# Kernel optimization log

Measured on AMD Instinct MI355X. Metric: run time of the kernel, lower is better.

## Reference

```python
import jax, jax.numpy as jnp
import numpy as np

DIM = 33
LAMBDA_SMOOTH = 1e-4
LAMBDA_MN = 10.0


def _tvmn(LUT):
    """TVMN smoothness/monotonicity regularizer on LUT [num,3,d,d,d]."""
    d = DIM
    edge = jnp.array([0, d - 2])
    wr = jnp.ones((d, d, d - 1), jnp.float32).at[..., edge].set(2.0)
    wg = jnp.ones((d, d - 1, d), jnp.float32).at[:, edge, :].set(2.0)
    wb = jnp.ones((d - 1, d, d), jnp.float32).at[edge, :, :].set(2.0)
    dif_r = LUT[..., :-1] - LUT[..., 1:]
    dif_g = LUT[..., :-1, :] - LUT[..., 1:, :]
    dif_b = LUT[..., :-1, :, :] - LUT[..., 1:, :, :]
    t0 = (dif_r ** 2 * wr).mean() + (dif_g ** 2 * wg).mean() + (dif_b ** 2 * wb).mean()
    t1 = ((jax.nn.relu(dif_r * wr)) ** 2).mean() \
       + ((jax.nn.relu(dif_g * wg)) ** 2).mean() \
       + ((jax.nn.relu(dif_b * wb)) ** 2).mean()
    return LAMBDA_SMOOTH * t0 + LAMBDA_MN * t1


def _trilinear_one(lut, img):
    """lut: [3,d,d,d] indexed [c, b_idx, g_idx, r_idx]; img: [3,H,W] in [0,1).
    Matches the CUDA kernel: id = r_id + g_id*dim + b_id*dim^2 per channel."""
    d = DIM
    binsize = 1.000001 / (d - 1)
    r, g, b = img[0], img[1], img[2]
    fr = r / binsize
    fg = g / binsize
    fb = b / binsize
    rid = jnp.floor(fr).astype(jnp.int32)
    gid = jnp.floor(fg).astype(jnp.int32)
    bid = jnp.floor(fb).astype(jnp.int32)
    rd = fr - rid  # fractional parts
    gd = fg - gid
    bd = fb - bid

    def corner(db, dg, dr):
        return lut[:, bid + db, gid + dg, rid + dr]  # [3,H,W]

    out = ((1 - rd) * (1 - gd) * (1 - bd)) * corner(0, 0, 0) \
        + (rd * (1 - gd) * (1 - bd)) * corner(0, 0, 1) \
        + ((1 - rd) * gd * (1 - bd)) * corner(0, 1, 0) \
        + (rd * gd * (1 - bd)) * corner(0, 1, 1) \
        + ((1 - rd) * (1 - gd) * bd) * corner(1, 0, 0) \
        + (rd * (1 - gd) * bd) * corner(1, 0, 1) \
        + ((1 - rd) * gd * bd) * corner(1, 1, 0) \
        + (rd * gd * bd) * corner(1, 1, 1)
    return out  # [3,H,W]


def setup_inputs() -> dict:
    key = jax.random.key(0)
    k1, k2, k3 = jax.random.split(key, 3)
    B, num, d = 4, 20, DIM
    weights = jax.random.normal(k1, (B, num), jnp.float32)
    LUTs = jax.random.normal(k2, (num, 3, d, d, d), jnp.float32) * 0.1
    img_org = jax.random.uniform(k3, (B, 3, 1080, 1920), jnp.float32)
    return {"weights": weights, "LUTs": LUTs, "img_org": img_org}


def reference(weights, LUTs, img_org):
    # CLUT mode '--': D3LUTs = LUTs directly; TVMN regularizer on the bases
    tvmn_loss = _tvmn(LUTs)
    num = LUTs.shape[0]
    # weights.mm(D3LUTs.reshape(num,-1)).reshape(-1,3,d,d,d)
    D3LUT = jnp.einsum('bn,ncijk->bcijk', weights, LUTs)  # [B,3,d,d,d]
    # per-batch LUT trilinear interpolation (lut.shape[0]==x.shape[0] branch)
    img_res = jax.vmap(_trilinear_one)(D3LUT, img_org)  # [B,3,H,W]
    fakes = img_res + img_org
    return (fakes, D3LUT, tvmn_loss)
```

## Files before the change

### kernel.cpp

```cpp
#include <hip/hip_runtime.h>
#include <hip/hip_fp16.h>

#define DIM 33
#define D2  (DIM*DIM)
#define D3  (DIM*DIM*DIM)
#define CH3 (3*D3)
#define NUM 20
#define BATCH 4
#define IMG_H 1080
#define IMG_W 1920
#define HW (IMG_H*IMG_W)
#define FAKES_SIZE (BATCH*3*HW)
#define D3LUT_SIZE (BATCH*CH3)
#define NCELL 32
#define CELLS (NCELL*NCELL*NCELL)
#define TVMN_BLOCKS 2112
#define TEX_BYTES ((size_t)BATCH * CELLS * 32)
#define PX_PER_BLOCK 512
#define TRI_PIX_BLOCKS (BATCH * HW / PX_PER_BLOCK)

typedef unsigned int u32x4 __attribute__((ext_vector_type(4)));

__global__ void mix_tvmn_kernel(const float* __restrict__ w,
                                const float* __restrict__ luts,
                                float* __restrict__ d3lut,
                                float* __restrict__ partials) {
    int t = blockIdx.x * blockDim.x + threadIdx.x;

    if (t < CH3) {
        float a0 = 0.f, a1 = 0.f, a2 = 0.f, a3 = 0.f;
#pragma unroll
        for (int n = 0; n < NUM; ++n) {
            float v = luts[(size_t)n * CH3 + t];
            a0 += w[0 * NUM + n] * v;
            a1 += w[1 * NUM + n] * v;
            a2 += w[2 * NUM + n] * v;
            a3 += w[3 * NUM + n] * v;
        }
        d3lut[(size_t)0 * CH3 + t] = a0;
        d3lut[(size_t)1 * CH3 + t] = a1;
        d3lut[(size_t)2 * CH3 + t] = a2;
        d3lut[(size_t)3 * CH3 + t] = a3;
    }

    const int total = NUM * 3 * D3;
    float s0 = 0.f, s1 = 0.f;
    for (int idx = t; idx < total; idx += gridDim.x * blockDim.x) {
        int k  = idx % DIM;
        int r1 = idx / DIM;
        int j  = r1 % DIM;
        int r2 = r1 / DIM;
        int i  = r2 % DIM;
        float v = luts[idx];
        if (k < DIM - 1) {
            float dif = v - luts[idx + 1];
            float ww = (k == 0 || k == DIM - 2) ? 2.f : 1.f;
            s0 += ww * dif * dif;
            float rp = dif > 0.f ? dif : 0.f;
            s1 += (ww * rp) * (ww * rp);
        }
        if (j < DIM - 1) {
            float dif = v - luts[idx + DIM];
            float ww = (j == 0 || j == DIM - 2) ? 2.f : 1.f;
            s0 += ww * dif * dif;
            float rp = dif > 0.f ? dif : 0.f;
            s1 += (ww * rp) * (ww * rp);
        }
        if (i < DIM - 1) {
            float dif = v - luts[idx + D2];
            float ww = (i == 0 || i == DIM - 2) ? 2.f : 1.f;
            s0 += ww * dif * dif;
            float rp = dif > 0.f ? dif : 0.f;
            s1 += (ww * rp) * (ww * rp);
        }
    }
#pragma unroll
    for (int off = 32; off > 0; off >>= 1) {
        s0 += __shfl_down(s0, off, 64);
        s1 += __shfl_down(s1, off, 64);
    }
    __shared__ float sh0[4], sh1[4];
    int wid = threadIdx.x >> 6, lane = threadIdx.x & 63;
    if (lane == 0) { sh0[wid] = s0; sh1[wid] = s1; }
    __syncthreads();
    if (threadIdx.x == 0) {
        partials[2 * blockIdx.x]     = sh0[0] + sh0[1] + sh0[2] + sh0[3];
        partials[2 * blockIdx.x + 1] = sh1[0] + sh1[1] + sh1[2] + sh1[3];
    }
}

__global__ void pack_cell_kernel(const float* __restrict__ d3lut,
                                 unsigned int* __restrict__ tex) {
    int t = blockIdx.x * blockDim.x + threadIdx.x;
    if (t >= BATCH * CELLS) return;
    int b = t >> 15;
    int cidx = t & (CELLS - 1);
    int bid = cidx >> 10;
    int gid = (cidx >> 5) & 31;
    int rid = cidx & 31;
    const float* L = d3lut + (size_t)b * CH3 + bid * D2 + gid * DIM + rid;

    float v[24];
    float amax = 0.f;
#pragma unroll
    for (int cr = 0; cr < 8; ++cr) {
        int off = (cr >> 2) * D2 + ((cr >> 1) & 1) * DIM + (cr & 1);
#pragma unroll
        for (int c = 0; c < 3; ++c) {
            float val = L[(size_t)c * D3 + off];
            v[cr * 3 + c] = val;
            amax = fmaxf(amax, fabsf(val));
        }
    }
    float s = amax * (1.0f / 511.0f);
    __half sh = __float2half(s);
    float sf = __half2float(sh);
    float inv = sf > 0.f ? 1.0f / sf : 0.f;

    unsigned int wq[8] = {0, 0, 0, 0, 0, 0, 0, 0};
#pragma unroll
    for (int i = 0; i < 24; ++i) {
        int m = (int)rintf(v[i] * inv);
        m = m > 511 ? 511 : (m < -511 ? -511 : m);
        unsigned int u = (unsigned int)(m + 512);
        int li   = (i < 12) ? i : (i - 12);
        int base = (i < 12) ? 0 : 4;
        int off = 10 * li;
        int dw = base + (off >> 5), shl = off & 31;
        wq[dw] |= u << shl;
        if (shl > 22) wq[dw + 1] |= u >> (32 - shl);
    }
    unsigned int sc = (unsigned int)__half_as_ushort(sh);
    wq[3] |= (sc & 0xffu) << 24;
    wq[7] |= (sc >> 8) << 24;

    uint4* dst = reinterpret_cast<uint4*>(tex + (size_t)t * 8);
    dst[0] = make_uint4(wq[0], wq[1], wq[2], wq[3]);
    dst[1] = make_uint4(wq[4], wq[5], wq[6], wq[7]);
}

__device__ __forceinline__ int xcd_swizzle(int blk, int nwg) {
    int q = nwg >> 3, r = nwg & 7;
    int xcd = blk & 7, idx = blk >> 3;
    int base = (xcd < r) ? xcd * (q + 1) : r * (q + 1) + (xcd - r) * q;
    return base + idx;
}

__global__ void trilerp_pair_kernel(const float* __restrict__ img,
                                    const unsigned int* __restrict__ tex,
                                    float* __restrict__ out,
                                    const float* __restrict__ partials,
                                    float* __restrict__ loss) {
    int blk = xcd_swizzle(blockIdx.x, gridDim.x);

    if (blk >= TRI_PIX_BLOCKS) {
        float s0 = 0.f, s1 = 0.f;
        for (int i = threadIdx.x; i < TVMN_BLOCKS; i += blockDim.x) {
            s0 += partials[2 * i];
            s1 += partials[2 * i + 1];
        }
#pragma unroll
        for (int off = 32; off > 0; off >>= 1) {
            s0 += __shfl_down(s0, off, 64);
            s1 += __shfl_down(s1, off, 64);
        }
        __shared__ float sh0[4], sh1[4];
        int wid = threadIdx.x >> 6, lane = threadIdx.x & 63;
        if (lane == 0) { sh0[wid] = s0; sh1[wid] = s1; }
        __syncthreads();
        if (threadIdx.x == 0) {
            s0 = sh0[0] + sh0[1] + sh0[2] + sh0[3];
            s1 = sh1[0] + sh1[1] + sh1[2] + sh1[3];
            const float invN = 1.0f / (float)(NUM * 3 * DIM * DIM * (DIM - 1));
            *loss = (1e-4f * s0 + 10.0f * s1) * invN;
        }
        return;
    }

    const int lane_pair = threadIdx.x >> 1;
    const int par = threadIdx.x & 1;

    long base = (long)blk * PX_PER_BLOCK;
    int b = (int)(base / HW);
    int p0 = (int)(base - (long)b * HW);

    const float* im = img + (size_t)b * 3 * HW;
    float* o = out + (size_t)b * 3 * HW;
    const unsigned int* tb = tex + (size_t)b * CELLS * 8;

    const float INVBIN = (float)(DIM - 1) / 1.000001f;

#pragma unroll
    for (int rnd = 0; rnd < 4; ++rnd) {
        int p = p0 + rnd * 128 + lane_pair;

        float r  = im[p];
        float g  = im[HW + p];
        float bl = im[2 * HW + p];

        float fr = r * INVBIN, fg = g * INVBIN, fb = bl * INVBIN;
        int rid = (int)fr, gid = (int)fg, bid = (int)fb;
        float rd = fr - (float)rid;
        float gd = fg - (float)gid;
        float bd = fb - (float)bid;

        unsigned int cell = ((unsigned)bid * NCELL + (unsigned)gid) * NCELL
                            + (unsigned)rid;
        const u32x4* cp = reinterpret_cast<const u32x4*>(
            tb + (size_t)cell * 8 + par * 4);
        u32x4 q = *cp;
        unsigned int wd[4] = {q.x, q.y, q.z, q.w};

        unsigned int myb = wd[3] >> 24;
        unsigned int otb = __shfl_xor(myb, 1, 64);
        unsigned int su = par ? (otb | (myb << 8)) : (myb | (otb << 8));
        float s = __half2float(__ushort_as_half((unsigned short)su));

        float r0 = 1.f - rd, g0 = 1.f - gd;
        float bfac = par ? bd : (1.f - bd);
        float w0 = bfac * g0 * r0;
        float w1 = bfac * g0 * rd;
        float w2 = bfac * gd * r0;
        float w3 = bfac * gd * rd;

        float A0 = 0.f, A1 = 0.f, A2 = 0.f;
#pragma unroll
        for (int li = 0; li < 12; ++li) {
            int off = 10 * li;
            int dw = off >> 5, shl = off & 31;
            unsigned int u = wd[dw] >> shl;
            if (shl > 22) u |= wd[dw + 1] << (32 - shl);
            u &= 1023u;
            float uf = (float)u;
            float wgt = (li < 3) ? w0 : (li < 6) ? w1 : (li < 9) ? w2 : w3;
            int c = li - (li / 3) * 3;
            if (c == 0) A0 += wgt * uf;
            else if (c == 1) A1 += wgt * uf;
            else A2 += wgt * uf;
        }
        A0 += __shfl_xor(A0, 1, 64);
        A1 += __shfl_xor(A1, 1, 64);
        A2 += __shfl_xor(A2, 1, 64);

        if (par == 0) {
            float nb = -512.f * s;
            __builtin_nontemporal_store(fmaf(s, A0, nb) + r,  o + p);
            __builtin_nontemporal_store(fmaf(s, A1, nb) + g,  o + HW + p);
            __builtin_nontemporal_store(fmaf(s, A2, nb) + bl, o + 2 * HW + p);
        }
    }
}

__global__ void tvmn_atomic_kernel(const float* __restrict__ luts,
                                   float* __restrict__ loss) {
    const int total = NUM * 3 * D3;
    float s0 = 0.f, s1 = 0.f;
    for (int idx = blockIdx.x * blockDim.x + threadIdx.x; idx < total;
         idx += gridDim.x * blockDim.x) {
        int k  = idx % DIM;
        int r1 = idx / DIM;
        int j  = r1 % DIM;
        int r2 = r1 / DIM;
        int i  = r2 % DIM;
        float v = luts[idx];
        if (k < DIM - 1) {
            float dif = v - luts[idx + 1];
            float ww = (k == 0 || k == DIM - 2) ? 2.f : 1.f;
            s0 += ww * dif * dif;
            float rp = dif > 0.f ? dif : 0.f;
            s1 += (ww * rp) * (ww * rp);
        }
        if (j < DIM - 1) {
            float dif = v - luts[idx + DIM];
            float ww = (j == 0 || j == DIM - 2) ? 2.f : 1.f;
            s0 += ww * dif * dif;
            float rp = dif > 0.f ? dif : 0.f;
            s1 += (ww * rp) * (ww * rp);
        }
        if (i < DIM - 1) {
            float dif = v - luts[idx + D2];
            float ww = (i == 0 || i == DIM - 2) ? 2.f : 1.f;
            s0 += ww * dif * dif;
            float rp = dif > 0.f ? dif : 0.f;
            s1 += (ww * rp) * (ww * rp);
        }
    }
#pragma unroll
    for (int off = 32; off > 0; off >>= 1) {
        s0 += __shfl_down(s0, off, 64);
        s1 += __shfl_down(s1, off, 64);
    }
    __shared__ float sh0[4], sh1[4];
    int wid = threadIdx.x >> 6, lane = threadIdx.x & 63;
    if (lane == 0) { sh0[wid] = s0; sh1[wid] = s1; }
    __syncthreads();
    if (threadIdx.x == 0) {
        s0 = sh0[0] + sh0[1] + sh0[2] + sh0[3];
        s1 = sh1[0] + sh1[1] + sh1[2] + sh1[3];
        const float invN = 1.0f / (float)(NUM * 3 * DIM * DIM * (DIM - 1));
        atomicAdd(loss, (1e-4f * s0 + 10.0f * s1) * invN);
    }
}

__global__ void mix_lut_kernel(const float* __restrict__ w,
                               const float* __restrict__ luts,
                               float* __restrict__ d3lut,
                               float* __restrict__ loss) {
    int t = blockIdx.x * blockDim.x + threadIdx.x;
    if (t == 0) *loss = 0.f;
    if (t >= BATCH * CH3) return;
    int b = t / CH3;
    int i = t - b * CH3;
    float acc = 0.f;
#pragma unroll
    for (int n = 0; n < NUM; ++n)
        acc += w[b * NUM + n] * luts[(size_t)n * CH3 + i];
    d3lut[t] = acc;
}

__global__ void trilerp_kernel(const float* __restrict__ img,
                               const float* __restrict__ d3lut,
                               float* __restrict__ out) {
    int t = blockIdx.x * blockDim.x + threadIdx.x;
    if (t >= BATCH * HW) return;
    int b = t / HW;
    int p = t - b * HW;
    const float* im = img + (size_t)b * 3 * HW + p;
    float r = im[0], g = im[HW], bl = im[2 * HW];
    const float binsize = 1.000001f / (float)(DIM - 1);
    float fr = r / binsize, fg = g / binsize, fb = bl / binsize;
    int rid = (int)fr, gid = (int)fg, bid = (int)fb;
    float rd = fr - rid, gd = fg - gid, bd = fb - bid;
    float w000 = (1.f - rd) * (1.f - gd) * (1.f - bd);
    float w001 = rd * (1.f - gd) * (1.f - bd);
    float w010 = (1.f - rd) * gd * (1.f - bd);
    float w011 = rd * gd * (1.f - bd);
    float w100 = (1.f - rd) * (1.f - gd) * bd;
    float w101 = rd * (1.f - gd) * bd;
    float w110 = (1.f - rd) * gd * bd;
    float w111 = rd * gd * bd;
    const float* lut = d3lut + (size_t)b * CH3;
    int base = bid * D2 + gid * DIM + rid;
    float* o = out + (size_t)b * 3 * HW + p;
#pragma unroll
    for (int c = 0; c < 3; ++c) {
        const float* l = lut + (size_t)c * D3 + base;
        float v = w000 * l[0]        + w001 * l[1]
                + w010 * l[DIM]      + w011 * l[DIM + 1]
                + w100 * l[D2]       + w101 * l[D2 + 1]
                + w110 * l[D2 + DIM] + w111 * l[D2 + DIM + 1];
        o[c * HW] = v + im[c * HW];
    }
}

extern "C" void kernel_launch(void* const* d_in, const int* in_sizes, int n_in,
                              void* d_out, int out_size, void* d_ws, size_t ws_size,
                              hipStream_t stream) {
    const float* weights = (const float*)d_in[0];
    const float* luts    = (const float*)d_in[1];
    const float* img     = (const float*)d_in[2];

    float* out   = (float*)d_out;
    float* fakes = out;
    float* d3lut = out + FAKES_SIZE;
    float* loss  = out + FAKES_SIZE + D3LUT_SIZE;

    const size_t need = TEX_BYTES + (size_t)TVMN_BLOCKS * 2 * sizeof(float);
    if (ws_size >= need) {
        unsigned int* tex = (unsigned int*)d_ws;
        float* partials = (float*)((char*)d_ws + TEX_BYTES);

        mix_tvmn_kernel<<<TVMN_BLOCKS, 256, 0, stream>>>(weights, luts, d3lut,
                                                         partials);
        pack_cell_kernel<<<(BATCH * CELLS + 255) / 256, 256, 0, stream>>>(d3lut,
                                                                          tex);
        trilerp_pair_kernel<<<TRI_PIX_BLOCKS + 1, 256, 0, stream>>>(
            img, tex, fakes, partials, loss);
    } else {
        mix_lut_kernel<<<(BATCH * CH3 + 255) / 256, 256, 0, stream>>>(
            weights, luts, d3lut, loss);
        tvmn_atomic_kernel<<<2112, 256, 0, stream>>>(luts, loss);
        int npix = BATCH * HW;
        trilerp_kernel<<<(npix + 255) / 256, 256, 0, stream>>>(img, d3lut, fakes);
    }
}
```

Baseline: 70.73 us.

## Move TVMN regularizer into trilerp kernel to overlap with pixel work

Moves the TVMN smoothness reduction out of the first mix kernel and into 1024 extra leading blocks of the trilinear interpolation kernel, each reducing its share and atomically adding into the loss. The mix kernel now only computes the blended LUT and zeroes the loss, so it runs with far fewer blocks and shortens the serial chain before packing. The TVMN work then overlaps with the bandwidth-bound pixel pass. It adds float atomics, which make the loss summation order nondeterministic, and the TVMN blocks compete with pixel blocks for CUs.

Result: slower. 77.26 us (+9.2%).

```diff
diff --git a/kernel.cpp b/kernel.cpp
--- a/kernel.cpp
+++ b/kernel.cpp
@@ -14,79 +14,34 @@
 #define D3LUT_SIZE (BATCH*CH3)
 #define NCELL 32
 #define CELLS (NCELL*NCELL*NCELL)
-#define TVMN_BLOCKS 2112
 #define TEX_BYTES ((size_t)BATCH * CELLS * 32)
 #define PX_PER_BLOCK 512
 #define TRI_PIX_BLOCKS (BATCH * HW / PX_PER_BLOCK)
+#define TVMN_XBLOCKS 1024
+#define TRI_TOTAL_BLOCKS (TVMN_XBLOCKS + TRI_PIX_BLOCKS)
 
 typedef unsigned int u32x4 __attribute__((ext_vector_type(4)));
 
-__global__ void mix_tvmn_kernel(const float* __restrict__ w,
-                                const float* __restrict__ luts,
-                                float* __restrict__ d3lut,
-                                float* __restrict__ partials) {
+__global__ void mix_kernel(const float* __restrict__ w,
+                           const float* __restrict__ luts,
+                           float* __restrict__ d3lut,
+                           float* __restrict__ loss) {
     int t = blockIdx.x * blockDim.x + threadIdx.x;
-
-    if (t < CH3) {
-        float a0 = 0.f, a1 = 0.f, a2 = 0.f, a3 = 0.f;
-#pragma unroll
-        for (int n = 0; n < NUM; ++n) {
-            float v = luts[(size_t)n * CH3 + t];
-            a0 += w[0 * NUM + n] * v;
-            a1 += w[1 * NUM + n] * v;
-            a2 += w[2 * NUM + n] * v;
-            a3 += w[3 * NUM + n] * v;
-        }
-        d3lut[(size_t)0 * CH3 + t] = a0;
-        d3lut[(size_t)1 * CH3 + t] = a1;
-        d3lut[(size_t)2 * CH3 + t] = a2;
-        d3lut[(size_t)3 * CH3 + t] = a3;
-    }
-
-    const int total = NUM * 3 * D3;
-    float s0 = 0.f, s1 = 0.f;
-    for (int idx = t; idx < total; idx += gridDim.x * blockDim.x) {
-        int k  = idx % DIM;
-        int r1 = idx / DIM;
-        int j  = r1 % DIM;
-        int r2 = r1 / DIM;
-        int i  = r2 % DIM;
-        float v = luts[idx];
-        if (k < DIM - 1) {
-            float dif = v - luts[idx + 1];
-            float ww = (k == 0 || k == DIM - 2) ? 2.f : 1.f;
-            s0 += ww * dif * dif;
-            float rp = dif > 0.f ? dif : 0.f;
-            s1 += (ww * rp) * (ww * rp);
-        }
-        if (j < DIM - 1) {
-            float dif = v - luts[idx + DIM];
-            float ww = (j == 0 || j == DIM - 2) ? 2.f : 1.f;
-            s0 += ww * dif * dif;
-            float rp = dif > 0.f ? dif : 0.f;
-            s1 += (ww * rp) * (ww * rp);
-        }
-        if (i < DIM - 1) {
-            float dif = v - luts[idx + D2];
-            float ww = (i == 0 || i == DIM - 2) ? 2.f : 1.f;
-            s0 += ww * dif * dif;
-            float rp = dif > 0.f ? dif : 0.f;
-            s1 += (ww * rp) * (ww * rp);
-        }
-    }
-#pragma unroll
-    for (int off = 32; off > 0; off >>= 1) {
-        s0 += __shfl_down(s0, off, 64);
-        s1 += __shfl_down(s1, off, 64);
-    }
-    __shared__ float sh0[4], sh1[4];
-    int wid = threadIdx.x >> 6, lane = threadIdx.x & 63;
-    if (lane == 0) { sh0[wid] = s0; sh1[wid] = s1; }
-    __syncthreads();
-    if (threadIdx.x == 0) {
-        partials[2 * blockIdx.x]     = sh0[0] + sh0[1] + sh0[2] + sh0[3];
-        partials[2 * blockIdx.x + 1] = sh1[0] + sh1[1] + sh1[2] + sh1[3];
-    }
+    if (t == 0) *loss = 0.f;
+    if (t >= CH3) return;
+    float a0 = 0.f, a1 = 0.f, a2 = 0.f, a3 = 0.f;
+#pragma unroll
+    for (int n = 0; n < NUM; ++n) {
+        float v = luts[(size_t)n * CH3 + t];
+        a0 += w[0 * NUM + n] * v;
+        a1 += w[1 * NUM + n] * v;
+        a2 += w[2 * NUM + n] * v;
+        a3 += w[3 * NUM + n] * v;
+    }
+    d3lut[(size_t)0 * CH3 + t] = a0;
+    d3lut[(size_t)1 * CH3 + t] = a1;
+    d3lut[(size_t)2 * CH3 + t] = a2;
+    d3lut[(size_t)3 * CH3 + t] = a3;
 }
 
 __global__ void pack_cell_kernel(const float* __restrict__ d3lut,
@@ -146,18 +101,43 @@
     return base + idx;
 }
 
-__global__ void trilerp_pair_kernel(const float* __restrict__ img,
+__global__ void trilerp_tvmn_kernel(const float* __restrict__ img,
                                     const unsigned int* __restrict__ tex,
                                     float* __restrict__ out,
-                                    const float* __restrict__ partials,
+                                    const float* __restrict__ luts,
                                     float* __restrict__ loss) {
-    int blk = xcd_swizzle(blockIdx.x, gridDim.x);
-
-    if (blk >= TRI_PIX_BLOCKS) {
+    if (blockIdx.x < TVMN_XBLOCKS) {
+        const int total = NUM * 3 * D3;
         float s0 = 0.f, s1 = 0.f;
-        for (int i = threadIdx.x; i < TVMN_BLOCKS; i += blockDim.x) {
-            s0 += partials[2 * i];
-            s1 += partials[2 * i + 1];
+        for (int idx = blockIdx.x * blockDim.x + threadIdx.x; idx < total;
+             idx += TVMN_XBLOCKS * blockDim.x) {
+            int k  = idx % DIM;
+            int r1 = idx / DIM;
+            int j  = r1 % DIM;
+            int r2 = r1 / DIM;
+            int i  = r2 % DIM;
+            float v = luts[idx];
+            if (k < DIM - 1) {
+                float dif = v - luts[idx + 1];
+                float ww = (k == 0 || k == DIM - 2) ? 2.f : 1.f;
+                s0 += ww * dif * dif;
+                float rp = dif > 0.f ? dif : 0.f;
+                s1 += (ww * rp) * (ww * rp);
+            }
+            if (j < DIM - 1) {
+                float dif = v - luts[idx + DIM];
+                float ww = (j == 0 || j == DIM - 2) ? 2.f : 1.f;
+                s0 += ww * dif * dif;
+                float rp = dif > 0.f ? dif : 0.f;
+                s1 += (ww * rp) * (ww * rp);
+            }
+            if (i < DIM - 1) {
+                float dif = v - luts[idx + D2];
+                float ww = (i == 0 || i == DIM - 2) ? 2.f : 1.f;
+                s0 += ww * dif * dif;
+                float rp = dif > 0.f ? dif : 0.f;
+                s1 += (ww * rp) * (ww * rp);
+            }
         }
 #pragma unroll
         for (int off = 32; off > 0; off >>= 1) {
@@ -172,10 +152,12 @@
             s0 = sh0[0] + sh0[1] + sh0[2] + sh0[3];
             s1 = sh1[0] + sh1[1] + sh1[2] + sh1[3];
             const float invN = 1.0f / (float)(NUM * 3 * DIM * DIM * (DIM - 1));
-            *loss = (1e-4f * s0 + 10.0f * s1) * invN;
+            atomicAdd(loss, (1e-4f * s0 + 10.0f * s1) * invN);
         }
         return;
     }
+
+    int blk = xcd_swizzle(blockIdx.x - TVMN_XBLOCKS, TRI_PIX_BLOCKS);
 
     const int lane_pair = threadIdx.x >> 1;
     const int par = threadIdx.x & 1;
@@ -365,17 +347,15 @@
     float* d3lut = out + FAKES_SIZE;
     float* loss  = out + FAKES_SIZE + D3LUT_SIZE;
 
-    const size_t need = TEX_BYTES + (size_t)TVMN_BLOCKS * 2 * sizeof(float);
-    if (ws_size >= need) {
+    if (ws_size >= TEX_BYTES) {
         unsigned int* tex = (unsigned int*)d_ws;
-        float* partials = (float*)((char*)d_ws + TEX_BYTES);
-
-        mix_tvmn_kernel<<<TVMN_BLOCKS, 256, 0, stream>>>(weights, luts, d3lut,
-                                                         partials);
+
+        mix_kernel<<<(CH3 + 255) / 256, 256, 0, stream>>>(weights, luts, d3lut,
+                                                          loss);
         pack_cell_kernel<<<(BATCH * CELLS + 255) / 256, 256, 0, stream>>>(d3lut,
                                                                           tex);
-        trilerp_pair_kernel<<<TRI_PIX_BLOCKS + 1, 256, 0, stream>>>(
-            img, tex, fakes, partials, loss);
+        trilerp_tvmn_kernel<<<TRI_TOTAL_BLOCKS, 256, 0, stream>>>(
+            img, tex, fakes, luts, loss);
     } else {
         mix_lut_kernel<<<(BATCH * CH3 + 255) / 256, 256, 0, stream>>>(
             weights, luts, d3lut, loss);
```
